# Kernel optimization log

Measured on AMD Instinct MI355X. Metric: run time of the kernel, lower is better.

## Reference

```python
import jax, jax.numpy as jnp
import numpy as np

PATCH = 16

def setup_inputs() -> dict:
    key = jax.random.key(0)
    k1, k2, k3, k4, k5 = jax.random.split(key, 5)
    B, C, H, W = 128, 3, 224, 224
    N = (H // PATCH) * (W // PATCH)  # 196
    D = 768
    x = jax.random.normal(k1, (B, C, H, W), dtype=jnp.float32)
    ys = jax.random.randint(k2, (B, N), 0, H - PATCH + 1, dtype=jnp.int64)
    xs = jax.random.randint(k3, (B, N), 0, W - PATCH + 1, dtype=jnp.int64)
    W_proj = jax.random.normal(k4, (D, C * PATCH * PATCH), dtype=jnp.float32) * 0.02
    b_proj = jax.random.normal(k5, (D,), dtype=jnp.float32) * 0.02
    return {"x": x, "ys": ys, "xs": xs, "W_proj": W_proj, "b_proj": b_proj}

def reference(x, ys, xs, W_proj, b_proj):
    # x: [B, C, H, W]; ys, xs: [B, N] top-left patch coords
    B, C, H, W = x.shape
    N = ys.shape[1]
    P = PATCH
    # flattened within-patch offsets: d[p] = dy*W + dx, shape [P*P]
    dy = jnp.arange(P)[:, None]
    dx = jnp.arange(P)[None, :]
    d = (dy * W + dx).reshape(-1)  # [P*P]
    base = ys * W + xs                         # [B, N]
    indices = base[:, :, None] + d[None, None, :]  # [B, N, P*P]
    indices = indices.reshape(B, N * P * P)
    # gather over flattened spatial dims for every channel
    x_flat = x.reshape(B, C, H * W)
    patches = jnp.take_along_axis(
        x_flat, indices[:, None, :].astype(jnp.int32), axis=2
    )  # [B, C, N*P*P]
    patches = patches.reshape(B, C, N, P * P)
    patches = patches.transpose(0, 2, 1, 3).reshape(B, N, C * P * P)  # [B, N, C*P*P]
    patch_tokens = jnp.einsum('bnf,df->bnd', patches, W_proj) + b_proj  # [B, N, D]
    patch_positions = jnp.stack([ys, xs], axis=-1)  # [B, N, 2]
    return (patch_tokens, patch_positions)
```

## Files before the change

### kernel.cpp

```cpp
#include <hip/hip_runtime.h>
#include <hip/hip_bf16.h>

#define B_IMG   128
#define CH      3
#define HW      224
#define NPATCH  196
#define TOKENS  25088
#define PATCH   16
#define FDIM    768
#define DDIM    768
#define TOKELEMS ((size_t)TOKENS * FDIM)
#define OUT_TOKENS ((size_t)TOKENS * DDIM)

#define GATHER_BLOCKS (TOKENS * (FDIM / 4) / 256)
#define WCONV_BLOCKS  ((DDIM * FDIM / 4) / 256)

typedef short short8 __attribute__((ext_vector_type(8)));
typedef float f32x4  __attribute__((ext_vector_type(4)));

static __device__ __forceinline__ unsigned short f2bf(float v) {
  unsigned u = __float_as_uint(v);
  unsigned r = u + 0x7fffu + ((u >> 16) & 1u);
  return (unsigned short)(r >> 16);
}

static __device__ __forceinline__ void gload16(const short* g, short* l) {
  __builtin_amdgcn_global_load_lds(
      (const __attribute__((address_space(1))) void*)g,
      (__attribute__((address_space(3))) void*)l,
      16, 0, 0);
}

__global__ __launch_bounds__(256) void prep_kernel(
    const float* __restrict__ x, const int* __restrict__ ys,
    const int* __restrict__ xs, const float* __restrict__ W,
    short* __restrict__ patches, short* __restrict__ Wbf,
    float* __restrict__ pos) {
  const int blk = blockIdx.x;
  if (blk < GATHER_BLOCKS) {
    int e   = blk * 256 + threadIdx.x;
    int tok = e / 192;
    int q   = e - tok * 192;
    int f   = q * 4;
    int b   = tok / NPATCH;
    int y   = ys[tok];
    int xc  = xs[tok];
    int c   = f >> 8;
    int rem = f & 255;
    int py  = rem >> 4;
    int px  = rem & 15;
    const float* src = x + ((size_t)(b * CH + c) * HW + (y + py)) * HW + xc + px;
    ushort4 o;
    o.x = f2bf(src[0]); o.y = f2bf(src[1]); o.z = f2bf(src[2]); o.w = f2bf(src[3]);
    *(ushort4*)&patches[(size_t)tok * FDIM + f] = o;
    if (q == 0) {
      pos[(size_t)tok * 2]     = (float)y;
      pos[(size_t)tok * 2 + 1] = (float)xc;
    }
  } else {
    int i = ((blk - GATHER_BLOCKS) * 256 + threadIdx.x) * 4;
    float4 v = *(const float4*)&W[i];
    ushort4 o;
    o.x = f2bf(v.x); o.y = f2bf(v.y); o.z = f2bf(v.z); o.w = f2bf(v.w);
    *(ushort4*)&Wbf[i] = o;
  }
}

__global__ __launch_bounds__(512) void gemm_kernel(
    const short* __restrict__ A,
    const short* __restrict__ Bw,
    const float* __restrict__ bias,
    float* __restrict__ C) {
  __shared__ short As[4][256 * 32];
  __shared__ short Bs[4][128 * 32];

  const int tid = threadIdx.x;
  const int w   = tid >> 6;
  const int l   = tid & 63;
  const int wr  = w >> 1;
  const int wc  = w & 1;
  const int lr  = l & 15;
  const int lg  = l >> 4;

  const int id   = blockIdx.x;
  const int xcd  = id & 7;
  const int chnk = id >> 3;
  const int nid  = (xcd < 4 ? xcd * 74 : 4 * 74 + (xcd - 4) * 73) + chnk;
  const int mt   = nid / 6;
  const int nt   = nid - mt * 6;
  const int m0   = mt * 256;
  const int n0   = nt * 128;

  f32x4 acc[4][4];
  const f32x4 z = {0.f, 0.f, 0.f, 0.f};
#pragma unroll
  for (int mi = 0; mi < 4; ++mi)
#pragma unroll
    for (int ni = 0; ni < 4; ++ni) acc[mi][ni] = z;

  float bs[4];
#pragma unroll
  for (int ni = 0; ni < 4; ++ni)
    bs[ni] = bias[n0 + wc * 64 + ni * 16 + lr];
#pragma unroll
  for (int ni = 0; ni < 4; ++ni) asm volatile("" : "+v"(bs[ni]));

  const short* gA = A  + (size_t)(m0 + wr * 64 + wc * 32 + (l >> 2)) * FDIM + ((l & 3) << 3);
  const short* gB = Bw + (size_t)(n0 + wc * 64 + wr * 16 + (l >> 2)) * FDIM + ((l & 3) << 3);
  const int lAoff = (wr * 64 + wc * 32) * 32;
  const int lBoff = (wc * 64 + wr * 16) * 32;

  auto stage = [&](int slot, int s) {
    const int ko = s * 32;
    short* lA = &As[slot][lAoff];
    short* lB = &Bs[slot][lBoff];
    gload16(gA + ko, lA);
    gload16(gA + 16 * FDIM + ko, lA + 16 * 32);
    gload16(gB + ko, lB);
  };
  auto compute = [&](int slot) {
    const short* Ab = As[slot];
    const short* Bb = Bs[slot];
    short8 a[4], b[4];
    const int koff = lg * 8;
#pragma unroll
    for (int mi = 0; mi < 4; ++mi)
      a[mi] = *(const short8*)&Ab[(wr * 64 + mi * 16 + lr) * 32 + koff];
#pragma unroll
    for (int ni = 0; ni < 4; ++ni)
      b[ni] = *(const short8*)&Bb[(wc * 64 + ni * 16 + lr) * 32 + koff];
    __builtin_amdgcn_s_setprio(1);
#pragma unroll
    for (int mi = 0; mi < 4; ++mi)
#pragma unroll
      for (int ni = 0; ni < 4; ++ni)
        acc[mi][ni] =
            __builtin_amdgcn_mfma_f32_16x16x32_bf16(a[mi], b[ni], acc[mi][ni], 0, 0, 0);
    __builtin_amdgcn_s_setprio(0);
  };

  stage(0, 0);
  stage(1, 1);
  stage(2, 2);

  for (int s = 0; s < 21; ++s) {
    stage((s + 3) & 3, s + 3);
    asm volatile("s_waitcnt vmcnt(9)" ::: "memory");
    __builtin_amdgcn_s_barrier();
    compute(s & 3);
    __builtin_amdgcn_s_barrier();
  }
  asm volatile("s_waitcnt vmcnt(6)" ::: "memory");
  __builtin_amdgcn_s_barrier();
  compute(21 & 3);
  __builtin_amdgcn_s_barrier();
  asm volatile("s_waitcnt vmcnt(3)" ::: "memory");
  __builtin_amdgcn_s_barrier();
  compute(22 & 3);
  __builtin_amdgcn_s_barrier();
  asm volatile("s_waitcnt vmcnt(0)" ::: "memory");
  __builtin_amdgcn_s_barrier();
  compute(23 & 3);

#pragma unroll
  for (int ni = 0; ni < 4; ++ni) {
    const int col = n0 + wc * 64 + ni * 16 + lr;
#pragma unroll
    for (int mi = 0; mi < 4; ++mi) {
      const int row = m0 + wr * 64 + mi * 16 + lg * 4;
      const f32x4 v = acc[mi][ni];
#pragma unroll
      for (int j = 0; j < 4; ++j)
        C[(size_t)(row + j) * DDIM + col] = v[j] + bs[ni];
    }
  }
}

__global__ __launch_bounds__(256) void naive_kernel(
    const float* __restrict__ x, const int* __restrict__ ys,
    const int* __restrict__ xs, const float* __restrict__ W,
    const float* __restrict__ bias, float* __restrict__ out) {
  __shared__ float prow[FDIM];
  const int tok = blockIdx.x;
  const int t   = threadIdx.x;
  const int b   = tok / NPATCH;
  const int y   = ys[tok];
  const int xc  = xs[tok];
  for (int i = t; i < FDIM; i += 256) {
    int c = i >> 8, rem = i & 255, py = rem >> 4, px = rem & 15;
    prow[i] = x[((size_t)(b * CH + c) * HW + y + py) * HW + xc + px];
  }
  __syncthreads();
  for (int dd = 0; dd < 3; ++dd) {
    const int d = t + dd * 256;
    float s = bias[d];
    const float4* wr = (const float4*)&W[(size_t)d * FDIM];
    const float4* pr = (const float4*)prow;
    for (int f4 = 0; f4 < FDIM / 4; ++f4) {
      float4 wv = wr[f4];
      float4 pv = pr[f4];
      s += wv.x * pv.x + wv.y * pv.y + wv.z * pv.z + wv.w * pv.w;
    }
    out[(size_t)tok * DDIM + d] = s;
  }
  if (t == 0) {
    float* pos = out + OUT_TOKENS;
    pos[(size_t)tok * 2]     = (float)y;
    pos[(size_t)tok * 2 + 1] = (float)xc;
  }
}

extern "C" void kernel_launch(void* const* d_in, const int* in_sizes, int n_in,
                              void* d_out, int out_size, void* d_ws, size_t ws_size,
                              hipStream_t stream) {
  const float* x    = (const float*)d_in[0];
  const int*   ys   = (const int*)d_in[1];
  const int*   xs   = (const int*)d_in[2];
  const float* W    = (const float*)d_in[3];
  const float* bias = (const float*)d_in[4];
  float* out = (float*)d_out;
  float* pos = out + OUT_TOKENS;

  const size_t w_bytes = (size_t)DDIM * FDIM * 2;
  const size_t p_bytes = TOKELEMS * 2;
  if (ws_size >= w_bytes + p_bytes) {
    short* Wbf     = (short*)d_ws;
    short* patches = (short*)d_ws + (size_t)DDIM * FDIM;
    prep_kernel<<<GATHER_BLOCKS + WCONV_BLOCKS, 256, 0, stream>>>(
        x, ys, xs, W, patches, Wbf, pos);
    gemm_kernel<<<(TOKENS / 256) * (DDIM / 128), 512, 0, stream>>>(
        patches, Wbf, bias, out);
  } else {
    naive_kernel<<<TOKENS, 256, 0, stream>>>(x, ys, xs, W, bias, out);
  }
}
```

Baseline: 93.65 us.

## Enlarge GEMM tile to 256x256 with K=64 staging and interleaved MFMA pipeline

The bf16 GEMM now uses 256x256 output tiles with 8 waves in a 2x4 layout, 64-wide K slices in double-buffered LDS with an XOR swizzle, and a hand-scheduled ping-pong. The global-to-LDS loads for the next tiles are spread across four MFMA phases separated by barriers. The larger tile halves the number of blocks and raises arithmetic intensity per LDS load, and the swizzle targets LDS bank conflicts. The cost is more accumulator registers (128 floats per lane), fewer blocks (294) for wave balance across CUs, and an intricate barrier schedule that is easy to get wrong.

```diff
diff --git a/kernel.cpp b/kernel.cpp
--- a/kernel.cpp
+++ b/kernel.cpp
@@ -66,37 +66,33 @@
   }
 }
 
-__global__ __launch_bounds__(512) void gemm_kernel(
+#define MF(ACC, AF, BF) \
+  ACC = __builtin_amdgcn_mfma_f32_16x16x32_bf16(AF, BF, ACC, 0, 0, 0)
+
+__global__ __launch_bounds__(512, 2) void gemm_kernel(
     const short* __restrict__ A,
     const short* __restrict__ Bw,
     const float* __restrict__ bias,
     float* __restrict__ C) {
-  __shared__ short As[4][256 * 32];
-  __shared__ short Bs[4][128 * 32];
+  __shared__ short As[2][2][128 * 64];
+  __shared__ short Bs[2][2][128 * 64];
 
   const int tid = threadIdx.x;
   const int w   = tid >> 6;
   const int l   = tid & 63;
-  const int wr  = w >> 1;
-  const int wc  = w & 1;
+  const int wr  = w >> 2;
+  const int wc  = w & 3;
   const int lr  = l & 15;
   const int lg  = l >> 4;
 
   const int id   = blockIdx.x;
   const int xcd  = id & 7;
   const int chnk = id >> 3;
-  const int nid  = (xcd < 4 ? xcd * 74 : 4 * 74 + (xcd - 4) * 73) + chnk;
-  const int mt   = nid / 6;
-  const int nt   = nid - mt * 6;
+  const int nid  = (xcd < 6 ? xcd * 37 : 6 * 37 + (xcd - 6) * 36) + chnk;
+  const int mt   = nid / 3;
+  const int nt   = nid - mt * 3;
   const int m0   = mt * 256;
-  const int n0   = nt * 128;
-
-  f32x4 acc[4][4];
-  const f32x4 z = {0.f, 0.f, 0.f, 0.f};
-#pragma unroll
-  for (int mi = 0; mi < 4; ++mi)
-#pragma unroll
-    for (int ni = 0; ni < 4; ++ni) acc[mi][ni] = z;
+  const int n0   = nt * 256;
 
   float bs[4];
 #pragma unroll
@@ -105,69 +101,157 @@
 #pragma unroll
   for (int ni = 0; ni < 4; ++ni) asm volatile("" : "+v"(bs[ni]));
 
-  const short* gA = A  + (size_t)(m0 + wr * 64 + wc * 32 + (l >> 2)) * FDIM + ((l & 3) << 3);
-  const short* gB = Bw + (size_t)(n0 + wc * 64 + wr * 16 + (l >> 2)) * FDIM + ((l & 3) << 3);
-  const int lAoff = (wr * 64 + wc * 32) * 32;
-  const int lBoff = (wc * 64 + wr * 16) * 32;
-
-  auto stage = [&](int slot, int s) {
-    const int ko = s * 32;
-    short* lA = &As[slot][lAoff];
-    short* lB = &Bs[slot][lBoff];
-    gload16(gA + ko, lA);
-    gload16(gA + 16 * FDIM + ko, lA + 16 * 32);
-    gload16(gB + ko, lB);
-  };
-  auto compute = [&](int slot) {
-    const short* Ab = As[slot];
-    const short* Bb = Bs[slot];
-    short8 a[4], b[4];
-    const int koff = lg * 8;
+  f32x4 acc[8][4];
+  const f32x4 z = {0.f, 0.f, 0.f, 0.f};
+#pragma unroll
+  for (int mi = 0; mi < 8; ++mi)
+#pragma unroll
+    for (int ni = 0; ni < 4; ++ni) acc[mi][ni] = z;
+
+  const int srow = w * 8 + (l >> 3);
+  const int scol = ((l & 7) * 8) ^ (((l >> 5) & 1) * 16);
+  auto stA = [&](int buf, int half, int kt) {
+    const short* src = A + (size_t)(m0 + half * 128 + srow) * FDIM + kt * 64 + scol;
+    short* dst = &As[buf][half][(w * 8) * 64];
+    gload16(src, dst);
+    gload16(src + 64 * FDIM, dst + 64 * 64);
+  };
+  auto stB = [&](int buf, int half, int kt) {
+    const short* src = Bw + (size_t)(n0 + half * 128 + srow) * FDIM + kt * 64 + scol;
+    short* dst = &Bs[buf][half][(w * 8) * 64];
+    gload16(src, dst);
+    gload16(src + 64 * FDIM, dst + 64 * 64);
+  };
+
+  const int rk0 = (lg * 8) ^ ((lr & 4) ? 16 : 0);
+  const int rk1 = (32 + lg * 8) ^ ((lr & 4) ? 16 : 0);
+  auto rdA = [&](int buf, int mi, int ks) {
+    return *(const short8*)&As[buf][wr][(mi * 16 + lr) * 64 + (ks ? rk1 : rk0)];
+  };
+  auto rdB = [&](int buf, int ni, int ks) {
+    return *(const short8*)&Bs[buf][wc >> 1]
+        [((wc & 1) * 64 + ni * 16 + lr) * 64 + (ks ? rk1 : rk0)];
+  };
+
+  short8 af[4][2], ag[4][2], bf[4][2];
+
+  auto tile = [&](int t, int c, int cn, bool sA_, bool sBCD) {
+#pragma unroll
+    for (int mi = 0; mi < 4; ++mi) {
+      af[mi][0] = rdA(c, mi, 0); af[mi][1] = rdA(c, mi, 1);
+    }
+    if (wc < 2) {
+#pragma unroll
+      for (int ni = 0; ni < 4; ++ni) {
+        bf[ni][0] = rdB(c, ni, 0); bf[ni][1] = rdB(c, ni, 1);
+      }
+    } else {
+#pragma unroll
+      for (int ni = 0; ni < 2; ++ni) {
+        bf[ni][0] = rdB(c, ni, 0); bf[ni][1] = rdB(c, ni, 1);
+      }
+    }
+    if (sA_) stB(cn, 1, t + 1);
+    __builtin_amdgcn_s_barrier();
+    asm volatile("s_waitcnt lgkmcnt(0)" ::: "memory");
+    __builtin_amdgcn_sched_barrier(0);
+    __builtin_amdgcn_s_setprio(1);
 #pragma unroll
     for (int mi = 0; mi < 4; ++mi)
-      a[mi] = *(const short8*)&Ab[(wr * 64 + mi * 16 + lr) * 32 + koff];
-#pragma unroll
-    for (int ni = 0; ni < 4; ++ni)
-      b[ni] = *(const short8*)&Bb[(wc * 64 + ni * 16 + lr) * 32 + koff];
+#pragma unroll
+      for (int ni = 0; ni < 2; ++ni) {
+        MF(acc[mi][ni], af[mi][0], bf[ni][0]);
+        MF(acc[mi][ni], af[mi][1], bf[ni][1]);
+      }
+    __builtin_amdgcn_s_setprio(0);
+    __builtin_amdgcn_s_barrier();
+    __builtin_amdgcn_sched_barrier(0);
+#pragma unroll
+    for (int mi = 0; mi < 4; ++mi) {
+      ag[mi][0] = rdA(c, mi + 4, 0); ag[mi][1] = rdA(c, mi + 4, 1);
+    }
+    if (wc >= 2) {
+#pragma unroll
+      for (int ni = 2; ni < 4; ++ni) {
+        bf[ni][0] = rdB(c, ni, 0); bf[ni][1] = rdB(c, ni, 1);
+      }
+    }
+    if (sBCD) stB(c, 0, t + 2);
+    __builtin_amdgcn_s_barrier();
+    asm volatile("s_waitcnt lgkmcnt(0)" ::: "memory");
+    __builtin_amdgcn_sched_barrier(0);
     __builtin_amdgcn_s_setprio(1);
 #pragma unroll
     for (int mi = 0; mi < 4; ++mi)
 #pragma unroll
-      for (int ni = 0; ni < 4; ++ni)
-        acc[mi][ni] =
-            __builtin_amdgcn_mfma_f32_16x16x32_bf16(a[mi], b[ni], acc[mi][ni], 0, 0, 0);
+      for (int ni = 0; ni < 2; ++ni) {
+        MF(acc[mi + 4][ni], ag[mi][0], bf[ni][0]);
+        MF(acc[mi + 4][ni], ag[mi][1], bf[ni][1]);
+      }
     __builtin_amdgcn_s_setprio(0);
-  };
-
-  stage(0, 0);
-  stage(1, 1);
-  stage(2, 2);
-
-  for (int s = 0; s < 21; ++s) {
-    stage((s + 3) & 3, s + 3);
-    asm volatile("s_waitcnt vmcnt(9)" ::: "memory");
-    __builtin_amdgcn_s_barrier();
-    compute(s & 3);
-    __builtin_amdgcn_s_barrier();
-  }
+    __builtin_amdgcn_s_barrier();
+    __builtin_amdgcn_sched_barrier(0);
+    if (sBCD) stA(c, 0, t + 2);
+    __builtin_amdgcn_s_barrier();
+    __builtin_amdgcn_s_setprio(1);
+#pragma unroll
+    for (int mi = 0; mi < 4; ++mi)
+#pragma unroll
+      for (int ni = 2; ni < 4; ++ni) {
+        MF(acc[mi][ni], af[mi][0], bf[ni][0]);
+        MF(acc[mi][ni], af[mi][1], bf[ni][1]);
+      }
+    __builtin_amdgcn_s_setprio(0);
+    __builtin_amdgcn_s_barrier();
+    __builtin_amdgcn_sched_barrier(0);
+    if (sBCD) stA(c, 1, t + 2);
+    __builtin_amdgcn_s_barrier();
+    __builtin_amdgcn_s_setprio(1);
+#pragma unroll
+    for (int mi = 0; mi < 4; ++mi)
+#pragma unroll
+      for (int ni = 2; ni < 4; ++ni) {
+        MF(acc[mi + 4][ni], ag[mi][0], bf[ni][0]);
+        MF(acc[mi + 4][ni], ag[mi][1], bf[ni][1]);
+      }
+    __builtin_amdgcn_s_setprio(0);
+  };
+
+  stB(0, 0, 0);
+  stA(0, 0, 0);
+  stA(0, 1, 0);
+  stB(0, 1, 0);
+  stB(1, 0, 1);
+  stA(1, 0, 1);
+  stA(1, 1, 1);
   asm volatile("s_waitcnt vmcnt(6)" ::: "memory");
   __builtin_amdgcn_s_barrier();
-  compute(21 & 3);
-  __builtin_amdgcn_s_barrier();
-  asm volatile("s_waitcnt vmcnt(3)" ::: "memory");
-  __builtin_amdgcn_s_barrier();
-  compute(22 & 3);
-  __builtin_amdgcn_s_barrier();
+  __builtin_amdgcn_sched_barrier(0);
+
+#pragma unroll 1
+  for (int tt = 0; tt < 5; ++tt) {
+    const int t0 = tt * 2;
+    tile(t0, 0, 1, true, true);
+    asm volatile("s_waitcnt vmcnt(6)" ::: "memory");
+    __builtin_amdgcn_s_barrier();
+    __builtin_amdgcn_sched_barrier(0);
+    tile(t0 + 1, 1, 0, true, true);
+    asm volatile("s_waitcnt vmcnt(6)" ::: "memory");
+    __builtin_amdgcn_s_barrier();
+    __builtin_amdgcn_sched_barrier(0);
+  }
+  tile(10, 0, 1, true, false);
   asm volatile("s_waitcnt vmcnt(0)" ::: "memory");
   __builtin_amdgcn_s_barrier();
-  compute(23 & 3);
+  __builtin_amdgcn_sched_barrier(0);
+  tile(11, 1, 0, false, false);
 
 #pragma unroll
   for (int ni = 0; ni < 4; ++ni) {
     const int col = n0 + wc * 64 + ni * 16 + lr;
 #pragma unroll
-    for (int mi = 0; mi < 4; ++mi) {
-      const int row = m0 + wr * 64 + mi * 16 + lg * 4;
+    for (int mi = 0; mi < 8; ++mi) {
+      const int row = m0 + wr * 128 + mi * 16 + lg * 4;
       const f32x4 v = acc[mi][ni];
 #pragma unroll
       for (int j = 0; j < 4; ++j)
@@ -228,7 +312,7 @@
     short* patches = (short*)d_ws + (size_t)DDIM * FDIM;
     prep_kernel<<<GATHER_BLOCKS + WCONV_BLOCKS, 256, 0, stream>>>(
         x, ys, xs, W, patches, Wbf, pos);
-    gemm_kernel<<<(TOKENS / 256) * (DDIM / 128), 512, 0, stream>>>(
+    gemm_kernel<<<(TOKENS / 256) * (DDIM / 256), 512, 0, stream>>>(
         patches, Wbf, bias, out);
   } else {
     naive_kernel<<<TOKENS, 256, 0, stream>>>(x, ys, xs, W, bias, out);
```

New measurement: 95.07 us. About the same (+1.5%).

## Reshape GEMM tile to 128x256 and double-buffer LDS fragment reads in registers

Applied to the files above, without the earlier changes.

The GEMM tile changes from 256x128 to 128x256, with a 2x4 wave grid and a 3-slot LDS ring instead of 4. The main loop now reads the next k-step's fragments from LDS into a second register set while MFMAs run on the current set. This is meant to hide LDS read latency behind MFMA work and to lower LDS use. The cost is higher VGPR pressure from the two fragment sets, and one fewer stage of global-load prefetch depth.

```diff
diff --git a/kernel.cpp b/kernel.cpp
--- a/kernel.cpp
+++ b/kernel.cpp
@@ -71,14 +71,14 @@
     const short* __restrict__ Bw,
     const float* __restrict__ bias,
     float* __restrict__ C) {
-  __shared__ short As[4][256 * 32];
-  __shared__ short Bs[4][128 * 32];
+  __shared__ short As[3][128 * 32];
+  __shared__ short Bs[3][256 * 32];
 
   const int tid = threadIdx.x;
   const int w   = tid >> 6;
   const int l   = tid & 63;
-  const int wr  = w >> 1;
-  const int wc  = w & 1;
+  const int wr  = w >> 2;
+  const int wc  = w & 3;
   const int lr  = l & 15;
   const int lg  = l >> 4;
 
@@ -86,10 +86,17 @@
   const int xcd  = id & 7;
   const int chnk = id >> 3;
   const int nid  = (xcd < 4 ? xcd * 74 : 4 * 74 + (xcd - 4) * 73) + chnk;
-  const int mt   = nid / 6;
-  const int nt   = nid - mt * 6;
-  const int m0   = mt * 256;
-  const int n0   = nt * 128;
+  const int mt   = nid / 3;
+  const int nt   = nid - mt * 3;
+  const int m0   = mt * 128;
+  const int n0   = nt * 256;
+
+  float bs[4];
+#pragma unroll
+  for (int ni = 0; ni < 4; ++ni)
+    bs[ni] = bias[n0 + wc * 64 + ni * 16 + lr];
+#pragma unroll
+  for (int ni = 0; ni < 4; ++ni) asm volatile("" : "+v"(bs[ni]));
 
   f32x4 acc[4][4];
   const f32x4 z = {0.f, 0.f, 0.f, 0.f};
@@ -98,69 +105,75 @@
 #pragma unroll
     for (int ni = 0; ni < 4; ++ni) acc[mi][ni] = z;
 
-  float bs[4];
-#pragma unroll
-  for (int ni = 0; ni < 4; ++ni)
-    bs[ni] = bias[n0 + wc * 64 + ni * 16 + lr];
-#pragma unroll
-  for (int ni = 0; ni < 4; ++ni) asm volatile("" : "+v"(bs[ni]));
-
-  const short* gA = A  + (size_t)(m0 + wr * 64 + wc * 32 + (l >> 2)) * FDIM + ((l & 3) << 3);
-  const short* gB = Bw + (size_t)(n0 + wc * 64 + wr * 16 + (l >> 2)) * FDIM + ((l & 3) << 3);
-  const int lAoff = (wr * 64 + wc * 32) * 32;
-  const int lBoff = (wc * 64 + wr * 16) * 32;
-
-  auto stage = [&](int slot, int s) {
-    const int ko = s * 32;
-    short* lA = &As[slot][lAoff];
-    short* lB = &Bs[slot][lBoff];
-    gload16(gA + ko, lA);
-    gload16(gA + 16 * FDIM + ko, lA + 16 * 32);
-    gload16(gB + ko, lB);
-  };
-  auto compute = [&](int slot) {
-    const short* Ab = As[slot];
-    const short* Bb = Bs[slot];
-    short8 a[4], b[4];
-    const int koff = lg * 8;
-#pragma unroll
-    for (int mi = 0; mi < 4; ++mi)
-      a[mi] = *(const short8*)&Ab[(wr * 64 + mi * 16 + lr) * 32 + koff];
-#pragma unroll
-    for (int ni = 0; ni < 4; ++ni)
-      b[ni] = *(const short8*)&Bb[(wc * 64 + ni * 16 + lr) * 32 + koff];
-    __builtin_amdgcn_s_setprio(1);
-#pragma unroll
-    for (int mi = 0; mi < 4; ++mi)
-#pragma unroll
-      for (int ni = 0; ni < 4; ++ni)
-        acc[mi][ni] =
-            __builtin_amdgcn_mfma_f32_16x16x32_bf16(a[mi], b[ni], acc[mi][ni], 0, 0, 0);
-    __builtin_amdgcn_s_setprio(0);
-  };
-
-  stage(0, 0);
-  stage(1, 1);
-  stage(2, 2);
-
-  for (int s = 0; s < 21; ++s) {
-    stage((s + 3) & 3, s + 3);
-    asm volatile("s_waitcnt vmcnt(9)" ::: "memory");
-    __builtin_amdgcn_s_barrier();
-    compute(s & 3);
-    __builtin_amdgcn_s_barrier();
-  }
+  const short* gA = A  + (size_t)(m0 + w * 16 + (l >> 2)) * FDIM + ((l & 3) << 3);
+  const short* gB = Bw + (size_t)(n0 + w * 32 + (l >> 2)) * FDIM + ((l & 3) << 3);
+  const int lA = (w * 16) * 32;
+  const int lB = (w * 32) * 32;
+
+  short8 f0[8], f1[8];
+
+#define STAGE(SLOT, KT)                                                   \
+  do {                                                                    \
+    const int ko_ = (KT) * 32;                                            \
+    gload16(gA + ko_, &As[(SLOT)][lA]);                                   \
+    gload16(gB + ko_, &Bs[(SLOT)][lB]);                                   \
+    gload16(gB + 16 * FDIM + ko_, &Bs[(SLOT)][lB + 16 * 32]);             \
+  } while (0)
+
+#define READF(SLOT, F)                                                    \
+  do {                                                                    \
+    const int rs_ = (SLOT);                                               \
+    _Pragma("unroll")                                                     \
+    for (int mi = 0; mi < 4; ++mi)                                        \
+      F[mi] = *(const short8*)&As[rs_][(wr * 64 + mi * 16 + lr) * 32 + lg * 8]; \
+    _Pragma("unroll")                                                     \
+    for (int ni = 0; ni < 4; ++ni)                                        \
+      F[4 + ni] = *(const short8*)&Bs[rs_][(wc * 64 + ni * 16 + lr) * 32 + lg * 8]; \
+  } while (0)
+
+#define MFMAC(F)                                                          \
+  do {                                                                    \
+    __builtin_amdgcn_s_setprio(1);                                        \
+    _Pragma("unroll")                                                     \
+    for (int mi = 0; mi < 4; ++mi)                                        \
+      _Pragma("unroll")                                                   \
+      for (int ni = 0; ni < 4; ++ni)                                      \
+        acc[mi][ni] = __builtin_amdgcn_mfma_f32_16x16x32_bf16(            \
+            F[mi], F[4 + ni], acc[mi][ni], 0, 0, 0);                      \
+    __builtin_amdgcn_s_setprio(0);                                        \
+  } while (0)
+
+#define STEP(S, CUR, NXT, DOSTAGE, VMIMM)                                 \
+  do {                                                                    \
+    if (DOSTAGE) STAGE((S) % 3, (S) + 3);                                 \
+    asm volatile("s_waitcnt vmcnt(" #VMIMM ")" ::: "memory");             \
+    __builtin_amdgcn_s_barrier();                                         \
+    READF(((S) + 1) % 3, NXT);                                            \
+    MFMAC(CUR);                                                           \
+    asm volatile("s_waitcnt lgkmcnt(0)" ::: "memory");                    \
+    __builtin_amdgcn_sched_barrier(0);                                    \
+    __builtin_amdgcn_s_barrier();                                         \
+  } while (0)
+
+  STAGE(0, 0);
+  STAGE(1, 1);
+  STAGE(2, 2);
   asm volatile("s_waitcnt vmcnt(6)" ::: "memory");
   __builtin_amdgcn_s_barrier();
-  compute(21 & 3);
+  READF(0, f0);
+  asm volatile("s_waitcnt lgkmcnt(0)" ::: "memory");
+  __builtin_amdgcn_sched_barrier(0);
   __builtin_amdgcn_s_barrier();
-  asm volatile("s_waitcnt vmcnt(3)" ::: "memory");
-  __builtin_amdgcn_s_barrier();
-  compute(22 & 3);
-  __builtin_amdgcn_s_barrier();
-  asm volatile("s_waitcnt vmcnt(0)" ::: "memory");
-  __builtin_amdgcn_s_barrier();
-  compute(23 & 3);
+
+#pragma unroll 1
+  for (int s = 0; s < 20; s += 2) {
+    STEP(s,     f0, f1, true, 6);
+    STEP(s + 1, f1, f0, true, 6);
+  }
+  STEP(20, f0, f1, true,  6);
+  STEP(21, f1, f0, false, 3);
+  STEP(22, f0, f1, false, 0);
+  MFMAC(f1);
 
 #pragma unroll
   for (int ni = 0; ni < 4; ++ni) {
@@ -174,6 +187,10 @@
         C[(size_t)(row + j) * DDIM + col] = v[j] + bs[ni];
     }
   }
+#undef STAGE
+#undef READF
+#undef MFMAC
+#undef STEP
 }
 
 __global__ __launch_bounds__(256) void naive_kernel(
@@ -228,7 +245,7 @@
     short* patches = (short*)d_ws + (size_t)DDIM * FDIM;
     prep_kernel<<<GATHER_BLOCKS + WCONV_BLOCKS, 256, 0, stream>>>(
         x, ys, xs, W, patches, Wbf, pos);
-    gemm_kernel<<<(TOKENS / 256) * (DDIM / 128), 512, 0, stream>>>(
+    gemm_kernel<<<(TOKENS / 128) * (DDIM / 256), 512, 0, stream>>>(
         patches, Wbf, bias, out);
   } else {
     naive_kernel<<<TOKENS, 256, 0, stream>>>(x, ys, xs, W, bias, out);
```

Result: slower. 101.2 us (+8.0%).
